# Kernel tuning notes

Measured on AMD Instinct MI355X. Metric: run time of the kernel, lower is better.

The kernel has to match this reference:

```python
import jax, jax.numpy as jnp
import numpy as np

B, T, H, WD = 512, 168, 512, 4  # batch, seq_len, hidden_dim, WEATHER_DIM


def setup_inputs() -> dict:
    key = jax.random.key(0)
    ks = jax.random.split(key, 11)
    sc = 1.0 / np.sqrt(H)

    def u(k, shape):
        return jax.random.uniform(k, shape, jnp.float32, -sc, sc)

    return {
        "inputs": jax.random.normal(ks[0], (B, T, WD + 1), dtype=jnp.float32),
        # layer 1: input_sz=1 (counts)
        "W1": u(ks[1], (1, 4 * H)),
        "U1": u(ks[2], (H, 4 * H)),
        "V1": u(ks[3], (WD, 4 * H)),
        "b1": u(ks[4], (4 * H,)),
        # layer 2: input_sz=H
        "W2": u(ks[5], (H, 4 * H)),
        "U2": u(ks[6], (H, 4 * H)),
        "V2": u(ks[7], (WD, 4 * H)),
        "b2": u(ks[8], (4 * H,)),
        # final linear head (xavier-ish init)
        "fc_w": u(ks[9], (1, H)),
        "fc_b": jnp.zeros((1,), jnp.float32),
    }


def pew_lstm(x, w, W, U, V, b):
    """Weather-conditioned LSTM layer.
    x: [B,T,I] main input, w: [B,T,WD] weather.
    Gates = x@W + h@U + weather@V + b (weather injected each step).
    Returns hidden sequence [B,T,H]."""
    bs = x.shape[0]
    hdim = U.shape[0]
    # precompute all non-recurrent contributions once: [B,T,4H]
    pre = jnp.einsum('bti,ig->btg', x, W) + jnp.einsum('btw,wg->btg', w, V) + b

    def step(carry, pre_t):
        h, c = carry
        gates = pre_t + h @ U              # [B,4H]
        i, f, g, o = jnp.split(gates, 4, axis=-1)
        c = jax.nn.sigmoid(f) * c + jax.nn.sigmoid(i) * jnp.tanh(g)
        h = jax.nn.sigmoid(o) * jnp.tanh(c)
        return (h, c), h

    h0 = jnp.zeros((bs, hdim), x.dtype)
    (_, _), hs = jax.lax.scan(step, (h0, h0), pre.transpose(1, 0, 2))
    return hs.transpose(1, 0, 2)  # [B,T,H]


def reference(inputs, W1, U1, V1, b1, W2, U2, V2, b2, fc_w, fc_b):
    weather = inputs[:, :, :-1]   # [B,T,WD]
    counts = inputs[:, :, -1:]    # [B,T,1]
    h1 = pew_lstm(counts, weather, W1, U1, V1, b1)
    h2 = pew_lstm(h1, weather, W2, U2, V2, b2)
    out = h2.reshape(-1, h2.shape[-1]) @ fc_w.T + fc_b  # [B*T,1]
    return out.reshape(-1)
```

## Files before the change

### kernel.cpp

```cpp
#include <hip/hip_runtime.h>
#include <cstdint>
#include <cstddef>

typedef unsigned int   u32;
typedef unsigned short u16;
typedef unsigned long long u64;
typedef __attribute__((ext_vector_type(8))) short bf16x8;
typedef __attribute__((ext_vector_type(4))) float f32x4;

#define B_  512
#define T_  168
#define H_  512

#define OFF_U1P   (0u)
#define OFF_UW2P  (2u*1024*1024)
#define OFF_FLAGS (6u*1024*1024)
#define OFF_H1    (8u*1024*1024)
#define OFF_H2    (12u*1024*1024)
#define H_SLOT    262144u
#define NRING     8
#define FS        32
#define SMEM_V9   (131072 + 6144 + 3072)

__device__ __forceinline__ u16 f2bf(float v){
  u32 u = __float_as_uint(v);
  return (u16)((u + 0x7fffu + ((u >> 16) & 1u)) >> 16);
}
__device__ __forceinline__ float sigm_f(float x){ return __fdividef(1.f, 1.f + __expf(-x)); }
__device__ __forceinline__ float tanh_ff(float x){
  float e = __expf(-2.f*fabsf(x));
  float t = __fdividef(1.f - e, 1.f + e);
  return (x < 0.f) ? -t : t;
}
__device__ __forceinline__ void async_cp16(const void* g, void* l){
  __builtin_amdgcn_global_load_lds((const __attribute__((address_space(1))) u32*)g,
                                   (__attribute__((address_space(3))) u32*)l, 16, 0, 0);
}


__device__ __forceinline__ void wpoll(const int* p, bool act, int target, int& vlast){
  if (__all((!act) || (vlast >= target))) return;
  while (true){
    int v = 0x7fffffff;
    if (act) v = __hip_atomic_load(p, __ATOMIC_RELAXED, __HIP_MEMORY_SCOPE_AGENT);
    if (__all(v >= target)){ vlast = v; break; }
    __builtin_amdgcn_s_sleep(1);
  }
}
template<bool PLAIN>
__device__ __forceinline__ bf16x8 ldh(const u16* p){
  if (PLAIN) return *(const bf16x8*)p;
  union { u64 q[2]; bf16x8 v; } u;
  u.q[0] = __hip_atomic_load((const u64*)p,     __ATOMIC_RELAXED, __HIP_MEMORY_SCOPE_AGENT);
  u.q[1] = __hip_atomic_load(((const u64*)p)+1, __ATOMIC_RELAXED, __HIP_MEMORY_SCOPE_AGENT);
  return u.v;
}
__device__ __forceinline__ void ring_st16(u16* p, uint4 v){
  u64 lo = ((u64)v.y << 32) | v.x;
  u64 hi = ((u64)v.w << 32) | v.z;
  __hip_atomic_store((u64*)p,     lo, __ATOMIC_RELAXED, __HIP_MEMORY_SCOPE_AGENT);
  __hip_atomic_store(((u64*)p)+1, hi, __ATOMIC_RELAXED, __HIP_MEMORY_SCOPE_AGENT);
}

__global__ void pack_w_kernel(const float* __restrict__ U1, const float* __restrict__ W2,
                              const float* __restrict__ U2, u16* __restrict__ U1p,
                              u16* __restrict__ UW2p)
{
  int idx = blockIdx.x*256 + threadIdx.x;
  int ln = idx & 63;
  int q8 = ((ln >> 4) << 3);
  int cl = ln & 15;
  if (idx < 16*128*64) {
    int kc = idx >> 13, ng = (idx >> 6) & 127;
    int row0 = kc*32 + q8, col = ng*16 + cl;
    u16* d = U1p + (size_t)idx*8;
    #pragma unroll
    for (int j=0;j<8;j++) d[j] = f2bf(U1[(size_t)(row0+j)*2048 + col]);
  } else {
    int i2 = idx - 16*128*64;
    if (i2 >= 32*128*64) return;
    int kc = i2 >> 13, ng = (i2 >> 6) & 127;
    int row0 = kc*32 + q8, col = ng*16 + cl;
    u16* d = UW2p + (size_t)i2*8;
    #pragma unroll
    for (int j=0;j<8;j++){
      int r = row0 + j;
      float v = (r < 512) ? W2[(size_t)r*2048 + col] : U2[(size_t)(r-512)*2048 + col];
      d[j] = f2bf(v);
    }
  }
}

__global__ void init_kernel(float* __restrict__ out, const float* __restrict__ fcb,
                            int* __restrict__ flags)
{
  int i = blockIdx.x*256 + threadIdx.x;
  if (i < 256*FS) flags[i] = 0;
  if (i < B_*T_) out[i] = fcb[0];
}

__device__ void run_l1(char* smem, int blk, const float* __restrict__ inp,
                       const float* __restrict__ W1, const float* __restrict__ V,
                       const float* __restrict__ bias, char* __restrict__ ws)
{
  u16*  Bl   = (u16*)smem;
  u16*  hlds = (u16*)(smem + 131072);
  float* wlds = (float*)(smem + 131072 + 6144);
  constexpr int RS = 40;
  const int tid = threadIdx.x, w = tid>>6, ln = tid&63, col = ln&15, quad = ln>>4;
  const int bi = blk & 7, hj = blk >> 3, h0 = hj*32, bg = bi*4 + w;

  const u16* Upak = (const u16*)(ws + OFF_U1P);
  const u16* H1r  = (const u16*)(ws + OFF_H1);
  u16* Hw = (u16*)(ws + OFF_H1);
  int* flag1 = (int*)(ws + OFF_FLAGS);
  int* flag2 = flag1 + 128*FS;
  const int* f1p = flag1 + (size_t)(bi*16 + (ln&15))*FS;
  const int* f2p = flag2 + (size_t)((bi>>1)*32 + (ln&31))*FS;
  int* myf = flag1 + (size_t)(bi*16 + hj)*FS;
  const bool a16 = ln < 16, a32 = ln < 32;
  int vl1 = 0, vlbp = 0;

  #pragma unroll
  for (int p=0;p<32;p++){
    int pid = w*32 + p, kc = pid>>3, ngl = pid&7;
    int ng = (ngl>>1)*32 + hj*2 + (ngl&1);
    async_cp16(Upak + ((size_t)(kc*128+ng)*64 + ln)*8, Bl + (size_t)pid*512);
  }
  for (int idx=tid; idx<4*32*6; idx+=256){
    int gate = idx/192, rem = idx%192, hcol = rem/6, k = rem%6;
    int gcol = gate*512 + h0 + hcol;
    wlds[idx] = (k==0)? bias[gcol] : (k<=4 ? V[(size_t)(k-1)*2048 + gcol] : W1[gcol]);
  }

  float c[8];
  #pragma unroll
  for (int i=0;i<8;i++) c[i] = 0.f;
  const f32x4 vzero = {0.f,0.f,0.f,0.f};

  for (int t=0; t<T_; t++){
    if (w == 0){
      if (t > 0)      wpoll(f1p, a16, t, vl1);
      if (t >= NRING) wpoll(f2p, a32, t-NRING+1, vlbp);
      __builtin_amdgcn_fence(__ATOMIC_ACQUIRE, "agent");
    }
    __syncthreads();

    f32x4 acc[8];
    #pragma unroll
    for (int i=0;i<8;i++) acc[i] = vzero;

    if (t > 0){
      const u16* ab = H1r + (size_t)((t-1)&7)*H_SLOT + (size_t)bg*16*512 + (size_t)ln*8;
      bf16x8 aw[8];
      #pragma unroll
      for (int i=0;i<8;i++) aw[i] = ldh<true>(ab + (size_t)i*512);
      #pragma unroll
      for (int kc=0; kc<16; kc++){
        bf16x8 av = aw[kc&7];
        if (kc < 8) aw[kc&7] = ldh<true>(ab + (size_t)(kc+8)*512);
        const u16* bb = Bl + (size_t)kc*8*512 + (size_t)ln*8;
        #pragma unroll
        for (int ngl=0; ngl<8; ngl++)
          acc[ngl] = __builtin_amdgcn_mfma_f32_16x16x32_bf16(
              av, *(const bf16x8*)(bb + (size_t)ngl*512), acc[ngl], 0,0,0);
      }
    }

    float iv[4][5];
    #pragma unroll
    for (int r=0;r<4;r++){
      const float* ip = inp + ((size_t)(bi*64 + w*16 + quad*4 + r)*T_ + t)*5;
      #pragma unroll
      for (int k=0;k<5;k++) iv[r][k] = ip[k];
    }
    #pragma unroll
    for (int hg=0; hg<2; hg++){
      float wv[4][6];
      #pragma unroll
      for (int gate=0; gate<4; gate++){
        const float* wp = wlds + (size_t)(gate*32 + hg*16 + col)*6;
        #pragma unroll
        for (int k=0;k<6;k++) wv[gate][k] = wp[k];
      }
      #pragma unroll
      for (int r=0;r<4;r++){
        float gv[4];
        #pragma unroll
        for (int gate=0; gate<4; gate++){
          gv[gate] = acc[gate*2+hg][r] + wv[gate][0]
                   + iv[r][0]*wv[gate][1] + iv[r][1]*wv[gate][2]
                   + iv[r][2]*wv[gate][3] + iv[r][3]*wv[gate][4]
                   + iv[r][4]*wv[gate][5];
        }
        float ig=sigm_f(gv[0]), fg=sigm_f(gv[1]), gg=tanh_ff(gv[2]), og=sigm_f(gv[3]);
        float cn = fg*c[hg*4+r] + ig*gg;
        c[hg*4+r] = cn;
        hlds[(size_t)(w*16 + quad*4 + r)*RS + hg*16 + col] = f2bf(og*tanh_ff(cn));
      }
    }
    {
      uint4 v = *(const uint4*)&hlds[(size_t)(w*16 + (ln&15))*RS + (ln>>4)*8];
      ring_st16(Hw + (size_t)(t&7)*H_SLOT + ((size_t)(bg*16 + hj)*64 + ln)*8, v);
    }
    __syncthreads();
    if (tid==0){
      __builtin_amdgcn_fence(__ATOMIC_RELEASE, "workgroup");
      __hip_atomic_store(myf, t+1, __ATOMIC_RELAXED, __HIP_MEMORY_SCOPE_AGENT);
    }
  }
}

template<bool PLAIN>
__device__ __forceinline__ void l2_half(f32x4* accA, f32x4* accB, const u16* Bh,
                                        const u16* A, int bgA, int bgB, int ln)
{
  const u16* pA = A + (size_t)bgA*16*512 + (size_t)ln*8;
  const u16* pB = A + (size_t)bgB*16*512 + (size_t)ln*8;
  bf16x8 awA[8], awB[8];
  #pragma unroll
  for (int i=0;i<8;i++){
    awA[i] = ldh<PLAIN>(pA + (size_t)i*512);
    awB[i] = ldh<PLAIN>(pB + (size_t)i*512);
  }
  #pragma unroll
  for (int kc=0; kc<16; kc++){
    bf16x8 avA = awA[kc&7], avB = awB[kc&7];
    if (kc < 8){
      awA[kc&7] = ldh<PLAIN>(pA + (size_t)(kc+8)*512);
      awB[kc&7] = ldh<PLAIN>(pB + (size_t)(kc+8)*512);
    }
    const u16* bb = Bh + (size_t)kc*4*512 + (size_t)ln*8;
    #pragma unroll
    for (int ngl=0; ngl<4; ngl++){
      bf16x8 bf = *(const bf16x8*)(bb + (size_t)ngl*512);
      accA[ngl] = __builtin_amdgcn_mfma_f32_16x16x32_bf16(avA, bf, accA[ngl], 0,0,0);
      accB[ngl] = __builtin_amdgcn_mfma_f32_16x16x32_bf16(avB, bf, accB[ngl], 0,0,0);
    }
  }
}

__device__ void run_l2(char* smem, int blk2, const float* __restrict__ inp,
                       const float* __restrict__ V, const float* __restrict__ bias,
                       const float* __restrict__ fcw, char* __restrict__ ws,
                       float* __restrict__ out)
{
  u16*  Bl   = (u16*)smem;
  u16*  hlds = (u16*)(smem + 131072);
  float* wlds = (float*)(smem + 131072 + 6144);
  constexpr int RS = 24;
  const int tid = threadIdx.x, w = tid>>6, ln = tid&63, col = ln&15, quad = ln>>4;
  const int bi2 = blk2 & 3, hj = blk2 >> 2, h0 = hj*16;
  const int bgA = bi2*8 + w, bgB = bgA + 4;

  const u16* Upak = (const u16*)(ws + OFF_UW2P);
  const u16* H1r  = (const u16*)(ws + OFF_H1);
  const u16* H2r  = (const u16*)(ws + OFF_H2);
  u16* Hw = (u16*)(ws + OFF_H2);
  int* flag1 = (int*)(ws + OFF_FLAGS);
  int* flag2 = flag1 + 128*FS;
  const int* h1f = flag1 + (size_t)(bi2*32 + (ln&31))*FS;
  const int* h2f = flag2 + (size_t)(bi2*32 + (ln&31))*FS;
  int* myf = flag2 + (size_t)(bi2*32 + hj)*FS;
  const bool a32 = ln < 32;
  int vlh1 = 0, vlh2 = 0;

  #pragma unroll
  for (int p=0;p<32;p++){
    int pid = w*32 + p, kc = pid>>2, ngl = pid&3;
    int ng = ngl*32 + hj;
    async_cp16(Upak + ((size_t)(kc*128+ng)*64 + ln)*8, Bl + (size_t)pid*512);
  }
  for (int idx=tid; idx<4*16*6; idx+=256){
    int gate = idx/96, rem = idx%96, hcol = rem/6, k = rem%6;
    int gcol = gate*512 + h0 + hcol;
    wlds[idx] = (k==0)? bias[gcol] : (k<=4 ? V[(size_t)(k-1)*2048 + gcol] : 0.f);
  }
  const float fcwr = fcw[h0 + col];

  float c[8];
  #pragma unroll
  for (int i=0;i<8;i++) c[i] = 0.f;
  const f32x4 vzero = {0.f,0.f,0.f,0.f};

  for (int t=0; t<T_; t++){
    if (w == 0){
      wpoll(h1f, a32, t+1, vlh1);
      __builtin_amdgcn_fence(__ATOMIC_ACQUIRE, "agent");
    }
    __syncthreads();

    f32x4 accA[4], accB[4];
    #pragma unroll
    for (int i=0;i<4;i++){ accA[i] = vzero; accB[i] = vzero; }

    const u16* A1 = H1r + (size_t)(t&7)*H_SLOT;
    l2_half<true>(accA, accB, Bl, A1, bgA, bgB, ln);

    if (t > 0){
      wpoll(h2f, a32, t, vlh2);
      __builtin_amdgcn_fence(__ATOMIC_ACQUIRE, "workgroup");
      const u16* A2 = H2r + (size_t)((t-1)&1)*H_SLOT;
      l2_half<false>(accA, accB, Bl + (size_t)16*4*512, A2, bgA, bgB, ln);
    }

    float wv[4][5];
    #pragma unroll
    for (int gate=0; gate<4; gate++){
      const float* wp = wlds + (size_t)(gate*16 + col)*6;
      #pragma unroll
      for (int k=0;k<5;k++) wv[gate][k] = wp[k];
    }
    float fcp[2][4];
    #pragma unroll
    for (int sel=0; sel<2; sel++){
      const f32x4* ac = sel ? accB : accA;
      #pragma unroll
      for (int r=0;r<4;r++){
        const float* ip = inp + ((size_t)(bi2*128 + sel*64 + w*16 + quad*4 + r)*T_ + t)*5;
        float i0=ip[0], i1=ip[1], i2=ip[2], i3=ip[3];
        float gv[4];
        #pragma unroll
        for (int gate=0; gate<4; gate++){
          gv[gate] = ac[gate][r] + wv[gate][0]
                   + i0*wv[gate][1] + i1*wv[gate][2] + i2*wv[gate][3] + i3*wv[gate][4];
        }
        float ig=sigm_f(gv[0]), fg=sigm_f(gv[1]), gg=tanh_ff(gv[2]), og=sigm_f(gv[3]);
        float cn = fg*c[sel*4+r] + ig*gg;
        c[sel*4+r] = cn;
        float h = og*tanh_ff(cn);
        fcp[sel][r] = h*fcwr;
        hlds[(size_t)(sel*64 + w*16 + quad*4 + r)*RS + col] = f2bf(h);
      }
    }
    {
      int sel = ln>>5, ch = (ln>>4)&1, m = ln&15;
      uint4 v = *(const uint4*)&hlds[(size_t)(sel*64 + w*16 + m)*RS + ch*8];
      int lp = ((hj&1)*2 + ch)*16 + m;
      int bgx = bi2*8 + sel*4 + w;
      ring_st16(Hw + (size_t)(t&1)*H_SLOT + ((size_t)(bgx*16 + (hj>>1))*64 + lp)*8, v);
    }
    __syncthreads();
    if (tid==0){
      __builtin_amdgcn_fence(__ATOMIC_RELEASE, "workgroup");
      __hip_atomic_store(myf, t+1, __ATOMIC_RELAXED, __HIP_MEMORY_SCOPE_AGENT);
    }

    #pragma unroll
    for (int sel=0; sel<2; sel++){
      #pragma unroll
      for (int r=0;r<4;r++){
        float v = fcp[sel][r];
        #pragma unroll
        for (int m=1;m<16;m<<=1) v += __shfl_xor(v, m, 16);
        if (col == 0)
          atomicAdd(&out[(size_t)(bi2*128 + sel*64 + w*16 + quad*4 + r)*T_ + t], v);
      }
    }
  }
}

__global__ void __launch_bounds__(256, 1)
lstm_main_v9(const float* __restrict__ inp, const float* __restrict__ W1,
             const float* __restrict__ V1, const float* __restrict__ b1,
             const float* __restrict__ V2, const float* __restrict__ b2,
             const float* __restrict__ fcw, char* __restrict__ ws, float* __restrict__ out)
{
  extern __shared__ char smem[];
  int blk = blockIdx.x;
  if (blk < 128) run_l1(smem, blk, inp, W1, V1, b1, ws);
  else           run_l2(smem, blk-128, inp, V2, b2, fcw, ws, out);
}

extern "C" void kernel_launch(void* const* d_in, const int* in_sizes, int n_in,
                              void* d_out, int out_size, void* d_ws, size_t ws_size,
                              hipStream_t stream) {
  (void)in_sizes; (void)n_in; (void)out_size; (void)ws_size;
  const float* inp = (const float*)d_in[0];
  const float* W1  = (const float*)d_in[1];
  const float* U1  = (const float*)d_in[2];
  const float* V1  = (const float*)d_in[3];
  const float* b1  = (const float*)d_in[4];
  const float* W2  = (const float*)d_in[5];
  const float* U2  = (const float*)d_in[6];
  const float* V2  = (const float*)d_in[7];
  const float* b2  = (const float*)d_in[8];
  const float* fcw = (const float*)d_in[9];
  const float* fcb = (const float*)d_in[10];
  char* ws = (char*)d_ws;
  float* out = (float*)d_out;

  pack_w_kernel<<<1536, 256, 0, stream>>>(U1, W2, U2,
      (u16*)(ws + OFF_U1P), (u16*)(ws + OFF_UW2P));
  init_kernel<<<(B_*T_ + 255)/256, 256, 0, stream>>>(out, fcb, (int*)(ws + OFF_FLAGS));

  (void)hipFuncSetAttribute((const void*)lstm_main_v9,
                            hipFuncAttributeMaxDynamicSharedMemorySize, SMEM_V9);
  lstm_main_v9<<<256, 256, SMEM_V9, stream>>>(inp, W1, V1, b1, V2, b2, fcw, ws, out);
}
```

Before: 2.222 ms.

## Store full hidden history and use per-wave flags instead of ring buffers

Replaces the 8-slot and 2-slot hidden-state ring buffers with full per-timestep history buffers in workspace, so layer 1 never waits on layer-2 back-pressure and the ring reuse constraint disappears. Synchronisation moves from block-wide barriers plus thread-0 flags to per-wave flags, with each wave draining its own stores and polling on its own, removing __syncthreads from the step loop. The old ring-based kernel stays as a fallback when the workspace is too small. The cost is much more workspace memory, more flag polling traffic, and reliance on relaxed per-wave ordering, which makes correctness harder to reason about.

Result: slower. 2.389 ms (+7.5%).

```diff
diff --git a/kernel.cpp b/kernel.cpp
--- a/kernel.cpp
+++ b/kernel.cpp
@@ -15,12 +15,16 @@
 #define OFF_U1P   (0u)
 #define OFF_UW2P  (2u*1024*1024)
 #define OFF_FLAGS (6u*1024*1024)
-#define OFF_H1    (8u*1024*1024)
-#define OFF_H2    (12u*1024*1024)
+#define OFF_H2R   (6u*1024*1024 + 512u*1024)
+#define OFF_H1_R9 (8u*1024*1024)
+#define OFF_H2_R9 (12u*1024*1024)
+#define OFF_H1F   (8u*1024*1024)
+#define SLOT_B    (524288u)
+#define OFF_H2F   (OFF_H1F + 168u*SLOT_B)
 #define H_SLOT    262144u
 #define NRING     8
 #define FS        32
-#define SMEM_V9   (131072 + 6144 + 3072)
+#define SMEM_SZ   (131072 + 6144 + 3072)
 
 __device__ __forceinline__ u16 f2bf(float v){
   u32 u = __float_as_uint(v);
@@ -36,8 +40,9 @@
   __builtin_amdgcn_global_load_lds((const __attribute__((address_space(1))) u32*)g,
                                    (__attribute__((address_space(3))) u32*)l, 16, 0, 0);
 }
-
-
+__device__ __forceinline__ void drain_vm(){
+  asm volatile("s_waitcnt vmcnt(0)" ::: "memory");
+}
 __device__ __forceinline__ void wpoll(const int* p, bool act, int target, int& vlast){
   if (__all((!act) || (vlast >= target))) return;
   while (true){
@@ -95,13 +100,43 @@
                             int* __restrict__ flags)
 {
   int i = blockIdx.x*256 + threadIdx.x;
-  if (i < 256*FS) flags[i] = 0;
+  if (i < 1024*FS) flags[i] = 0;
   if (i < B_*T_) out[i] = fcb[0];
 }
 
-__device__ void run_l1(char* smem, int blk, const float* __restrict__ inp,
-                       const float* __restrict__ W1, const float* __restrict__ V,
-                       const float* __restrict__ bias, char* __restrict__ ws)
+template<bool PLAIN>
+__device__ __forceinline__ void l2_half(f32x4* accA, f32x4* accB, const u16* Bh,
+                                        const u16* A, int bgA, int bgB, int ln)
+{
+  const u16* pA = A + (size_t)bgA*16*512 + (size_t)ln*8;
+  const u16* pB = A + (size_t)bgB*16*512 + (size_t)ln*8;
+  bf16x8 awA[8], awB[8];
+  #pragma unroll
+  for (int i=0;i<8;i++){
+    awA[i] = ldh<PLAIN>(pA + (size_t)i*512);
+    awB[i] = ldh<PLAIN>(pB + (size_t)i*512);
+  }
+  #pragma unroll
+  for (int kc=0; kc<16; kc++){
+    bf16x8 avA = awA[kc&7], avB = awB[kc&7];
+    if (kc < 8){
+      awA[kc&7] = ldh<PLAIN>(pA + (size_t)(kc+8)*512);
+      awB[kc&7] = ldh<PLAIN>(pB + (size_t)(kc+8)*512);
+    }
+    const u16* bb = Bh + (size_t)kc*4*512 + (size_t)ln*8;
+    #pragma unroll
+    for (int ngl=0; ngl<4; ngl++){
+      bf16x8 bf = *(const bf16x8*)(bb + (size_t)ngl*512);
+      accA[ngl] = __builtin_amdgcn_mfma_f32_16x16x32_bf16(avA, bf, accA[ngl], 0,0,0);
+      accB[ngl] = __builtin_amdgcn_mfma_f32_16x16x32_bf16(avB, bf, accB[ngl], 0,0,0);
+    }
+  }
+}
+
+
+__device__ void run_l1_fs(char* smem, int blk, const float* __restrict__ inp,
+                          const float* __restrict__ W1, const float* __restrict__ V,
+                          const float* __restrict__ bias, char* __restrict__ ws)
 {
   u16*  Bl   = (u16*)smem;
   u16*  hlds = (u16*)(smem + 131072);
@@ -111,15 +146,13 @@
   const int bi = blk & 7, hj = blk >> 3, h0 = hj*32, bg = bi*4 + w;
 
   const u16* Upak = (const u16*)(ws + OFF_U1P);
-  const u16* H1r  = (const u16*)(ws + OFF_H1);
-  u16* Hw = (u16*)(ws + OFF_H1);
+  const u16* H1f  = (const u16*)(ws + OFF_H1F);
+  u16* Hw = (u16*)(ws + OFF_H1F);
   int* flag1 = (int*)(ws + OFF_FLAGS);
-  int* flag2 = flag1 + 128*FS;
-  const int* f1p = flag1 + (size_t)(bi*16 + (ln&15))*FS;
-  const int* f2p = flag2 + (size_t)((bi>>1)*32 + (ln&31))*FS;
-  int* myf = flag1 + (size_t)(bi*16 + hj)*FS;
-  const bool a16 = ln < 16, a32 = ln < 32;
-  int vl1 = 0, vlbp = 0;
+  const int* f1p = flag1 + (size_t)((bi*16 + (ln&15))*4 + w)*FS;
+  int* myf = flag1 + (size_t)((bi*16 + hj)*4 + w)*FS;
+  const bool a16 = ln < 16;
+  int vl1 = 0;
 
   #pragma unroll
   for (int p=0;p<32;p++){
@@ -138,20 +171,17 @@
   for (int i=0;i<8;i++) c[i] = 0.f;
   const f32x4 vzero = {0.f,0.f,0.f,0.f};
 
+  __syncthreads();
+
   for (int t=0; t<T_; t++){
-    if (w == 0){
-      if (t > 0)      wpoll(f1p, a16, t, vl1);
-      if (t >= NRING) wpoll(f2p, a32, t-NRING+1, vlbp);
-      __builtin_amdgcn_fence(__ATOMIC_ACQUIRE, "agent");
-    }
-    __syncthreads();
-
     f32x4 acc[8];
     #pragma unroll
     for (int i=0;i<8;i++) acc[i] = vzero;
 
     if (t > 0){
-      const u16* ab = H1r + (size_t)((t-1)&7)*H_SLOT + (size_t)bg*16*512 + (size_t)ln*8;
+      wpoll(f1p, a16, t, vl1);
+      __builtin_amdgcn_fence(__ATOMIC_ACQUIRE, "workgroup");
+      const u16* ab = H1f + (size_t)(t-1)*H_SLOT + (size_t)bg*16*512 + (size_t)ln*8;
       bf16x8 aw[8];
       #pragma unroll
       for (int i=0;i<8;i++) aw[i] = ldh<true>(ab + (size_t)i*512);
@@ -201,49 +231,19 @@
     }
     {
       uint4 v = *(const uint4*)&hlds[(size_t)(w*16 + (ln&15))*RS + (ln>>4)*8];
-      ring_st16(Hw + (size_t)(t&7)*H_SLOT + ((size_t)(bg*16 + hj)*64 + ln)*8, v);
-    }
-    __syncthreads();
-    if (tid==0){
-      __builtin_amdgcn_fence(__ATOMIC_RELEASE, "workgroup");
+      ring_st16(Hw + (size_t)t*H_SLOT + ((size_t)(bg*16 + hj)*64 + ln)*8, v);
+    }
+    drain_vm();
+    if (ln == 0)
       __hip_atomic_store(myf, t+1, __ATOMIC_RELAXED, __HIP_MEMORY_SCOPE_AGENT);
-    }
-  }
-}
-
-template<bool PLAIN>
-__device__ __forceinline__ void l2_half(f32x4* accA, f32x4* accB, const u16* Bh,
-                                        const u16* A, int bgA, int bgB, int ln)
-{
-  const u16* pA = A + (size_t)bgA*16*512 + (size_t)ln*8;
-  const u16* pB = A + (size_t)bgB*16*512 + (size_t)ln*8;
-  bf16x8 awA[8], awB[8];
-  #pragma unroll
-  for (int i=0;i<8;i++){
-    awA[i] = ldh<PLAIN>(pA + (size_t)i*512);
-    awB[i] = ldh<PLAIN>(pB + (size_t)i*512);
-  }
-  #pragma unroll
-  for (int kc=0; kc<16; kc++){
-    bf16x8 avA = awA[kc&7], avB = awB[kc&7];
-    if (kc < 8){
-      awA[kc&7] = ldh<PLAIN>(pA + (size_t)(kc+8)*512);
-      awB[kc&7] = ldh<PLAIN>(pB + (size_t)(kc+8)*512);
-    }
-    const u16* bb = Bh + (size_t)kc*4*512 + (size_t)ln*8;
-    #pragma unroll
-    for (int ngl=0; ngl<4; ngl++){
-      bf16x8 bf = *(const bf16x8*)(bb + (size_t)ngl*512);
-      accA[ngl] = __builtin_amdgcn_mfma_f32_16x16x32_bf16(avA, bf, accA[ngl], 0,0,0);
-      accB[ngl] = __builtin_amdgcn_mfma_f32_16x16x32_bf16(avB, bf, accB[ngl], 0,0,0);
-    }
-  }
-}
-
-__device__ void run_l2(char* smem, int blk2, const float* __restrict__ inp,
-                       const float* __restrict__ V, const float* __restrict__ bias,
-                       const float* __restrict__ fcw, char* __restrict__ ws,
-                       float* __restrict__ out)
+  }
+}
+
+template<bool H2F>
+__device__ void run_l2_fs(char* smem, int blk2, const float* __restrict__ inp,
+                          const float* __restrict__ V, const float* __restrict__ bias,
+                          const float* __restrict__ fcw, char* __restrict__ ws,
+                          float* __restrict__ out)
 {
   u16*  Bl   = (u16*)smem;
   u16*  hlds = (u16*)(smem + 131072);
@@ -254,14 +254,14 @@
   const int bgA = bi2*8 + w, bgB = bgA + 4;
 
   const u16* Upak = (const u16*)(ws + OFF_UW2P);
-  const u16* H1r  = (const u16*)(ws + OFF_H1);
-  const u16* H2r  = (const u16*)(ws + OFF_H2);
-  u16* Hw = (u16*)(ws + OFF_H2);
+  const u16* H1f  = (const u16*)(ws + OFF_H1F);
+  const u16* H2b  = (const u16*)(ws + (H2F ? OFF_H2F : OFF_H2R));
+  u16* Hw = (u16*)(ws + (H2F ? OFF_H2F : OFF_H2R));
   int* flag1 = (int*)(ws + OFF_FLAGS);
-  int* flag2 = flag1 + 128*FS;
-  const int* h1f = flag1 + (size_t)(bi2*32 + (ln&31))*FS;
-  const int* h2f = flag2 + (size_t)(bi2*32 + (ln&31))*FS;
-  int* myf = flag2 + (size_t)(bi2*32 + hj)*FS;
+  int* flag2 = flag1 + 512*FS;
+  const int* h1f = flag1 + (size_t)((bi2*32 + (ln&31))*4 + w)*FS;
+  const int* h2f = flag2 + (size_t)((bi2*32 + (ln&31))*4 + w)*FS;
+  int* myf = flag2 + (size_t)((bi2*32 + hj)*4 + w)*FS;
   const bool a32 = ln < 32;
   int vlh1 = 0, vlh2 = 0;
 
@@ -283,25 +283,23 @@
   for (int i=0;i<8;i++) c[i] = 0.f;
   const f32x4 vzero = {0.f,0.f,0.f,0.f};
 
+  __syncthreads();
+
   for (int t=0; t<T_; t++){
-    if (w == 0){
-      wpoll(h1f, a32, t+1, vlh1);
-      __builtin_amdgcn_fence(__ATOMIC_ACQUIRE, "agent");
-    }
-    __syncthreads();
-
     f32x4 accA[4], accB[4];
     #pragma unroll
     for (int i=0;i<4;i++){ accA[i] = vzero; accB[i] = vzero; }
 
-    const u16* A1 = H1r + (size_t)(t&7)*H_SLOT;
+    wpoll(h1f, a32, t+1, vlh1);
+    __builtin_amdgcn_fence(__ATOMIC_ACQUIRE, "workgroup");
+    const u16* A1 = H1f + (size_t)t*H_SLOT;
     l2_half<true>(accA, accB, Bl, A1, bgA, bgB, ln);
 
     if (t > 0){
       wpoll(h2f, a32, t, vlh2);
       __builtin_amdgcn_fence(__ATOMIC_ACQUIRE, "workgroup");
-      const u16* A2 = H2r + (size_t)((t-1)&1)*H_SLOT;
-      l2_half<false>(accA, accB, Bl + (size_t)16*4*512, A2, bgA, bgB, ln);
+      const u16* A2 = H2b + (H2F ? (size_t)(t-1)*H_SLOT : (size_t)((t-1)&1)*H_SLOT);
+      l2_half<H2F>(accA, accB, Bl + (size_t)16*4*512, A2, bgA, bgB, ln);
     }
 
     float wv[4][5];
@@ -338,6 +336,251 @@
       uint4 v = *(const uint4*)&hlds[(size_t)(sel*64 + w*16 + m)*RS + ch*8];
       int lp = ((hj&1)*2 + ch)*16 + m;
       int bgx = bi2*8 + sel*4 + w;
+      u16* dst = Hw + (H2F ? (size_t)t*H_SLOT : (size_t)(t&1)*H_SLOT)
+               + ((size_t)(bgx*16 + (hj>>1))*64 + lp)*8;
+      ring_st16(dst, v);
+    }
+    drain_vm();
+    if (ln == 0)
+      __hip_atomic_store(myf, t+1, __ATOMIC_RELAXED, __HIP_MEMORY_SCOPE_AGENT);
+
+    #pragma unroll
+    for (int sel=0; sel<2; sel++){
+      #pragma unroll
+      for (int r=0;r<4;r++){
+        float v = fcp[sel][r];
+        #pragma unroll
+        for (int m=1;m<16;m<<=1) v += __shfl_xor(v, m, 16);
+        if (col == 0)
+          atomicAdd(&out[(size_t)(bi2*128 + sel*64 + w*16 + quad*4 + r)*T_ + t], v);
+      }
+    }
+  }
+}
+
+template<bool H2F>
+__global__ void __launch_bounds__(256, 1)
+lstm_main_v10(const float* __restrict__ inp, const float* __restrict__ W1,
+              const float* __restrict__ V1, const float* __restrict__ b1,
+              const float* __restrict__ V2, const float* __restrict__ b2,
+              const float* __restrict__ fcw, char* __restrict__ ws, float* __restrict__ out)
+{
+  extern __shared__ char smem[];
+  int blk = blockIdx.x;
+  if (blk < 128) run_l1_fs(smem, blk, inp, W1, V1, b1, ws);
+  else           run_l2_fs<H2F>(smem, blk-128, inp, V2, b2, fcw, ws, out);
+}
+
+__device__ void run_l1_r9(char* smem, int blk, const float* __restrict__ inp,
+                          const float* __restrict__ W1, const float* __restrict__ V,
+                          const float* __restrict__ bias, char* __restrict__ ws)
+{
+  u16*  Bl   = (u16*)smem;
+  u16*  hlds = (u16*)(smem + 131072);
+  float* wlds = (float*)(smem + 131072 + 6144);
+  constexpr int RS = 40;
+  const int tid = threadIdx.x, w = tid>>6, ln = tid&63, col = ln&15, quad = ln>>4;
+  const int bi = blk & 7, hj = blk >> 3, h0 = hj*32, bg = bi*4 + w;
+
+  const u16* Upak = (const u16*)(ws + OFF_U1P);
+  const u16* H1r  = (const u16*)(ws + OFF_H1_R9);
+  u16* Hw = (u16*)(ws + OFF_H1_R9);
+  int* flag1 = (int*)(ws + OFF_FLAGS);
+  int* flag2 = flag1 + 128*FS;
+  const int* f1p = flag1 + (size_t)(bi*16 + (ln&15))*FS;
+  const int* f2p = flag2 + (size_t)((bi>>1)*32 + (ln&31))*FS;
+  int* myf = flag1 + (size_t)(bi*16 + hj)*FS;
+  const bool a16 = ln < 16, a32 = ln < 32;
+  int vl1 = 0, vlbp = 0;
+
+  #pragma unroll
+  for (int p=0;p<32;p++){
+    int pid = w*32 + p, kc = pid>>3, ngl = pid&7;
+    int ng = (ngl>>1)*32 + hj*2 + (ngl&1);
+    async_cp16(Upak + ((size_t)(kc*128+ng)*64 + ln)*8, Bl + (size_t)pid*512);
+  }
+  for (int idx=tid; idx<4*32*6; idx+=256){
+    int gate = idx/192, rem = idx%192, hcol = rem/6, k = rem%6;
+    int gcol = gate*512 + h0 + hcol;
+    wlds[idx] = (k==0)? bias[gcol] : (k<=4 ? V[(size_t)(k-1)*2048 + gcol] : W1[gcol]);
+  }
+
+  float c[8];
+  #pragma unroll
+  for (int i=0;i<8;i++) c[i] = 0.f;
+  const f32x4 vzero = {0.f,0.f,0.f,0.f};
+
+  for (int t=0; t<T_; t++){
+    if (w == 0){
+      if (t > 0)      wpoll(f1p, a16, t, vl1);
+      if (t >= NRING) wpoll(f2p, a32, t-NRING+1, vlbp);
+      __builtin_amdgcn_fence(__ATOMIC_ACQUIRE, "agent");
+    }
+    __syncthreads();
+
+    f32x4 acc[8];
+    #pragma unroll
+    for (int i=0;i<8;i++) acc[i] = vzero;
+
+    if (t > 0){
+      const u16* ab = H1r + (size_t)((t-1)&7)*H_SLOT + (size_t)bg*16*512 + (size_t)ln*8;
+      bf16x8 aw[8];
+      #pragma unroll
+      for (int i=0;i<8;i++) aw[i] = ldh<true>(ab + (size_t)i*512);
+      #pragma unroll
+      for (int kc=0; kc<16; kc++){
+        bf16x8 av = aw[kc&7];
+        if (kc < 8) aw[kc&7] = ldh<true>(ab + (size_t)(kc+8)*512);
+        const u16* bb = Bl + (size_t)kc*8*512 + (size_t)ln*8;
+        #pragma unroll
+        for (int ngl=0; ngl<8; ngl++)
+          acc[ngl] = __builtin_amdgcn_mfma_f32_16x16x32_bf16(
+              av, *(const bf16x8*)(bb + (size_t)ngl*512), acc[ngl], 0,0,0);
+      }
+    }
+
+    float iv[4][5];
+    #pragma unroll
+    for (int r=0;r<4;r++){
+      const float* ip = inp + ((size_t)(bi*64 + w*16 + quad*4 + r)*T_ + t)*5;
+      #pragma unroll
+      for (int k=0;k<5;k++) iv[r][k] = ip[k];
+    }
+    #pragma unroll
+    for (int hg=0; hg<2; hg++){
+      float wv[4][6];
+      #pragma unroll
+      for (int gate=0; gate<4; gate++){
+        const float* wp = wlds + (size_t)(gate*32 + hg*16 + col)*6;
+        #pragma unroll
+        for (int k=0;k<6;k++) wv[gate][k] = wp[k];
+      }
+      #pragma unroll
+      for (int r=0;r<4;r++){
+        float gv[4];
+        #pragma unroll
+        for (int gate=0; gate<4; gate++){
+          gv[gate] = acc[gate*2+hg][r] + wv[gate][0]
+                   + iv[r][0]*wv[gate][1] + iv[r][1]*wv[gate][2]
+                   + iv[r][2]*wv[gate][3] + iv[r][3]*wv[gate][4]
+                   + iv[r][4]*wv[gate][5];
+        }
+        float ig=sigm_f(gv[0]), fg=sigm_f(gv[1]), gg=tanh_ff(gv[2]), og=sigm_f(gv[3]);
+        float cn = fg*c[hg*4+r] + ig*gg;
+        c[hg*4+r] = cn;
+        hlds[(size_t)(w*16 + quad*4 + r)*RS + hg*16 + col] = f2bf(og*tanh_ff(cn));
+      }
+    }
+    {
+      uint4 v = *(const uint4*)&hlds[(size_t)(w*16 + (ln&15))*RS + (ln>>4)*8];
+      ring_st16(Hw + (size_t)(t&7)*H_SLOT + ((size_t)(bg*16 + hj)*64 + ln)*8, v);
+    }
+    __syncthreads();
+    if (tid==0){
+      __builtin_amdgcn_fence(__ATOMIC_RELEASE, "workgroup");
+      __hip_atomic_store(myf, t+1, __ATOMIC_RELAXED, __HIP_MEMORY_SCOPE_AGENT);
+    }
+  }
+}
+
+__device__ void run_l2_r9(char* smem, int blk2, const float* __restrict__ inp,
+                          const float* __restrict__ V, const float* __restrict__ bias,
+                          const float* __restrict__ fcw, char* __restrict__ ws,
+                          float* __restrict__ out)
+{
+  u16*  Bl   = (u16*)smem;
+  u16*  hlds = (u16*)(smem + 131072);
+  float* wlds = (float*)(smem + 131072 + 6144);
+  constexpr int RS = 24;
+  const int tid = threadIdx.x, w = tid>>6, ln = tid&63, col = ln&15, quad = ln>>4;
+  const int bi2 = blk2 & 3, hj = blk2 >> 2, h0 = hj*16;
+  const int bgA = bi2*8 + w, bgB = bgA + 4;
+
+  const u16* Upak = (const u16*)(ws + OFF_UW2P);
+  const u16* H1r  = (const u16*)(ws + OFF_H1_R9);
+  const u16* H2r  = (const u16*)(ws + OFF_H2_R9);
+  u16* Hw = (u16*)(ws + OFF_H2_R9);
+  int* flag1 = (int*)(ws + OFF_FLAGS);
+  int* flag2 = flag1 + 128*FS;
+  const int* h1f = flag1 + (size_t)(bi2*32 + (ln&31))*FS;
+  const int* h2f = flag2 + (size_t)(bi2*32 + (ln&31))*FS;
+  int* myf = flag2 + (size_t)(bi2*32 + hj)*FS;
+  const bool a32 = ln < 32;
+  int vlh1 = 0, vlh2 = 0;
+
+  #pragma unroll
+  for (int p=0;p<32;p++){
+    int pid = w*32 + p, kc = pid>>2, ngl = pid&3;
+    int ng = ngl*32 + hj;
+    async_cp16(Upak + ((size_t)(kc*128+ng)*64 + ln)*8, Bl + (size_t)pid*512);
+  }
+  for (int idx=tid; idx<4*16*6; idx+=256){
+    int gate = idx/96, rem = idx%96, hcol = rem/6, k = rem%6;
+    int gcol = gate*512 + h0 + hcol;
+    wlds[idx] = (k==0)? bias[gcol] : (k<=4 ? V[(size_t)(k-1)*2048 + gcol] : 0.f);
+  }
+  const float fcwr = fcw[h0 + col];
+
+  float c[8];
+  #pragma unroll
+  for (int i=0;i<8;i++) c[i] = 0.f;
+  const f32x4 vzero = {0.f,0.f,0.f,0.f};
+
+  for (int t=0; t<T_; t++){
+    if (w == 0){
+      wpoll(h1f, a32, t+1, vlh1);
+      __builtin_amdgcn_fence(__ATOMIC_ACQUIRE, "agent");
+    }
+    __syncthreads();
+
+    f32x4 accA[4], accB[4];
+    #pragma unroll
+    for (int i=0;i<4;i++){ accA[i] = vzero; accB[i] = vzero; }
+
+    const u16* A1 = H1r + (size_t)(t&7)*H_SLOT;
+    l2_half<true>(accA, accB, Bl, A1, bgA, bgB, ln);
+
+    if (t > 0){
+      wpoll(h2f, a32, t, vlh2);
+      __builtin_amdgcn_fence(__ATOMIC_ACQUIRE, "workgroup");
+      const u16* A2 = H2r + (size_t)((t-1)&1)*H_SLOT;
+      l2_half<false>(accA, accB, Bl + (size_t)16*4*512, A2, bgA, bgB, ln);
+    }
+
+    float wv[4][5];
+    #pragma unroll
+    for (int gate=0; gate<4; gate++){
+      const float* wp = wlds + (size_t)(gate*16 + col)*6;
+      #pragma unroll
+      for (int k=0;k<5;k++) wv[gate][k] = wp[k];
+    }
+    float fcp[2][4];
+    #pragma unroll
+    for (int sel=0; sel<2; sel++){
+      const f32x4* ac = sel ? accB : accA;
+      #pragma unroll
+      for (int r=0;r<4;r++){
+        const float* ip = inp + ((size_t)(bi2*128 + sel*64 + w*16 + quad*4 + r)*T_ + t)*5;
+        float i0=ip[0], i1=ip[1], i2=ip[2], i3=ip[3];
+        float gv[4];
+        #pragma unroll
+        for (int gate=0; gate<4; gate++){
+          gv[gate] = ac[gate][r] + wv[gate][0]
+                   + i0*wv[gate][1] + i1*wv[gate][2] + i2*wv[gate][3] + i3*wv[gate][4];
+        }
+        float ig=sigm_f(gv[0]), fg=sigm_f(gv[1]), gg=tanh_ff(gv[2]), og=sigm_f(gv[3]);
+        float cn = fg*c[sel*4+r] + ig*gg;
+        c[sel*4+r] = cn;
+        float h = og*tanh_ff(cn);
+        fcp[sel][r] = h*fcwr;
+        hlds[(size_t)(sel*64 + w*16 + quad*4 + r)*RS + col] = f2bf(h);
+      }
+    }
+    {
+      int sel = ln>>5, ch = (ln>>4)&1, m = ln&15;
+      uint4 v = *(const uint4*)&hlds[(size_t)(sel*64 + w*16 + m)*RS + ch*8];
+      int lp = ((hj&1)*2 + ch)*16 + m;
+      int bgx = bi2*8 + sel*4 + w;
       ring_st16(Hw + (size_t)(t&1)*H_SLOT + ((size_t)(bgx*16 + (hj>>1))*64 + lp)*8, v);
     }
     __syncthreads();
@@ -368,14 +611,14 @@
 {
   extern __shared__ char smem[];
   int blk = blockIdx.x;
-  if (blk < 128) run_l1(smem, blk, inp, W1, V1, b1, ws);
-  else           run_l2(smem, blk-128, inp, V2, b2, fcw, ws, out);
+  if (blk < 128) run_l1_r9(smem, blk, inp, W1, V1, b1, ws);
+  else           run_l2_r9(smem, blk-128, inp, V2, b2, fcw, ws, out);
 }
 
 extern "C" void kernel_launch(void* const* d_in, const int* in_sizes, int n_in,
                               void* d_out, int out_size, void* d_ws, size_t ws_size,
                               hipStream_t stream) {
-  (void)in_sizes; (void)n_in; (void)out_size; (void)ws_size;
+  (void)in_sizes; (void)n_in; (void)out_size;
   const float* inp = (const float*)d_in[0];
   const float* W1  = (const float*)d_in[1];
   const float* U1  = (const float*)d_in[2];
@@ -394,7 +637,20 @@
       (u16*)(ws + OFF_U1P), (u16*)(ws + OFF_UW2P));
   init_kernel<<<(B_*T_ + 255)/256, 256, 0, stream>>>(out, fcb, (int*)(ws + OFF_FLAGS));
 
-  (void)hipFuncSetAttribute((const void*)lstm_main_v9,
-                            hipFuncAttributeMaxDynamicSharedMemorySize, SMEM_V9);
-  lstm_main_v9<<<256, 256, SMEM_V9, stream>>>(inp, W1, V1, b1, V2, b2, fcw, ws, out);
-}
+  const size_t need_h1f  = (size_t)OFF_H1F + (size_t)T_*SLOT_B;
+  const size_t need_both = (size_t)OFF_H2F + (size_t)T_*SLOT_B;
+
+  if (ws_size >= need_both) {
+    (void)hipFuncSetAttribute((const void*)lstm_main_v10<true>,
+                              hipFuncAttributeMaxDynamicSharedMemorySize, SMEM_SZ);
+    lstm_main_v10<true><<<256, 256, SMEM_SZ, stream>>>(inp, W1, V1, b1, V2, b2, fcw, ws, out);
+  } else if (ws_size >= need_h1f) {
+    (void)hipFuncSetAttribute((const void*)lstm_main_v10<false>,
+                              hipFuncAttributeMaxDynamicSharedMemorySize, SMEM_SZ);
+    lstm_main_v10<false><<<256, 256, SMEM_SZ, stream>>>(inp, W1, V1, b1, V2, b2, fcw, ws, out);
+  } else {
+    (void)hipFuncSetAttribute((const void*)lstm_main_v9,
+                              hipFuncAttributeMaxDynamicSharedMemorySize, SMEM_SZ);
+    lstm_main_v9<<<256, 256, SMEM_SZ, stream>>>(inp, W1, V1, b1, V2, b2, fcw, ws, out);
+  }
+}
```
